# Optimization experiments

Hardware: AMD Instinct MI355X
Metric: run time of the kernel (lower is better)

The kernel has to match this reference:

```python
import jax, jax.numpy as jnp
import numpy as np

N = 100000          # nodes
DEG = 32            # fixed in-degree (every node has a non-empty mailbox)
E = N * DEG         # edges
IN_DIM = 25         # node feature dim; 3 aggregators * 1 scaler * 25 = 75
OUT_DIM = 128
AGG_EPS = 1e-5      # PNA std aggregator epsilon
BN_EPS = 1e-5       # BatchNorm1d epsilon


def setup_inputs() -> dict:
    key = jax.random.key(0)
    k = jax.random.split(key, 6)
    h = jax.random.normal(k[0], (N, IN_DIM), dtype=jnp.float32)
    snorm_n = jax.random.uniform(k[1], (N, 1), dtype=jnp.float32)
    # every node appears exactly DEG times as a destination -> degree 32
    edge_dst = jnp.repeat(jnp.arange(N, dtype=jnp.int32), DEG)
    edge_src = jax.random.randint(k[2], (E,), 0, N, dtype=jnp.int32)
    # posttrans MLP (1 layer): Linear(75 -> 128), no final activation
    W = jax.random.normal(k[3], (3 * IN_DIM, OUT_DIM), dtype=jnp.float32) / np.sqrt(3 * IN_DIM)
    b = jnp.zeros((OUT_DIM,), dtype=jnp.float32)
    # BatchNorm1d affine params
    gamma = jnp.ones((OUT_DIM,), dtype=jnp.float32)
    beta = jnp.zeros((OUT_DIM,), dtype=jnp.float32)
    return {"h": h, "snorm_n": snorm_n, "edge_src": edge_src, "edge_dst": edge_dst,
            "W": W, "b": b, "gamma": gamma, "beta": beta}


def reference(h, snorm_n, edge_src, edge_dst, W, b, gamma, beta):
    # --- message: e = src node features (pretrans_edges + message_func) ---
    e = h[edge_src]                                   # [E, IN_DIM] irregular gather
    # --- reduce: mean / max / std over each destination's mailbox ---
    ones = jnp.ones((e.shape[0],), dtype=h.dtype)
    deg = jax.ops.segment_sum(ones, edge_dst, num_segments=N)
    deg = jnp.maximum(deg, 1.0)[:, None]              # [N, 1]
    s1 = jax.ops.segment_sum(e, edge_dst, num_segments=N)
    mean = s1 / deg                                   # aggregate_mean
    mx = jax.ops.segment_max(e, edge_dst, num_segments=N)  # aggregate_max
    s2 = jax.ops.segment_sum(e * e, edge_dst, num_segments=N)
    var = jax.nn.relu(s2 / deg - mean * mean)         # aggregate_var
    std = jnp.sqrt(var + AGG_EPS)                     # aggregate_std
    agg = jnp.concatenate([mean, mx, std], axis=1)    # [N, 75]; identity scaler only
    # --- posttrans MLP: single Linear(75 -> 128), last_activation='none' ---
    z = agg @ W + b                                   # [N, OUT_DIM]
    # --- graph norm ---
    z = z * snorm_n
    # --- BatchNorm1d (training mode: batch statistics, biased variance) ---
    mu = jnp.mean(z, axis=0)
    v = jnp.var(z, axis=0)
    z = (z - mu) / jnp.sqrt(v + BN_EPS) * gamma + beta
    # --- relu; residual disabled (in_dim != out_dim); dropout p=0.0 is no-op ---
    return jax.nn.relu(z)
```

## Files before the change

### kernel.cpp

```cpp
#include <hip/hip_runtime.h>
#include <hip/hip_bf16.h>

#define NN 100000
#define DEG 32
#define IN_DIM 25
#define AGG_DIM 75
#define KPAD 104
#define OUT_DIM 128
#define NPB 10
#define NCHUNK (NN / NPB)
#define BLK 256
#define GRID 2048

typedef __attribute__((ext_vector_type(8))) short short8;
typedef __attribute__((ext_vector_type(4))) float f32x4;

static __device__ __forceinline__ ushort f2bf(float x) {
    __hip_bfloat16 h = __float2bfloat16(x);
    return *reinterpret_cast<ushort*>(&h);
}
static __device__ __forceinline__ float bf2f(ushort u) {
    return __uint_as_float(((unsigned)u) << 16);
}

__global__ __launch_bounds__(BLK) void prep(const float4* __restrict__ h4,
                                            ushort4* __restrict__ hb4,
                                            float* __restrict__ bnbuf) {
    int i = blockIdx.x * BLK + threadIdx.x;
    if (i < 2 * OUT_DIM) bnbuf[i] = 0.0f;
    const int total = NN * IN_DIM / 4;
    for (; i < total; i += GRID * BLK) {
        float4 v = h4[i];
        ushort4 o;
        o.x = f2bf(v.x); o.y = f2bf(v.y); o.z = f2bf(v.z); o.w = f2bf(v.w);
        hb4[i] = o;
    }
}

__global__ __launch_bounds__(BLK) void pna_main(
    const ushort* __restrict__ hb, const float* __restrict__ snorm,
    const int* __restrict__ esrc, const float* __restrict__ W,
    const float* __restrict__ b, float* __restrict__ z,
    float* __restrict__ bnbuf)
{
    __shared__ ushort agg[16][KPAD];

    const int t = threadIdx.x;
    const int lane = t & 63;
    const int wv = t >> 6;

    for (int i = t; i < 16 * KPAD; i += BLK) ((ushort*)agg)[i] = 0;

    const int cb0 = (wv * 2 + 0) * 16 + (lane & 15);
    const int cb1 = (wv * 2 + 1) * 16 + (lane & 15);
    short8 bfrag[2][3];
    #pragma unroll
    for (int ct = 0; ct < 2; ++ct) {
        const int cb = ct ? cb1 : cb0;
        #pragma unroll
        for (int kt = 0; kt < 3; ++kt) {
            short8 fr;
            #pragma unroll
            for (int j = 0; j < 8; ++j) {
                const int k = kt * 32 + ((lane >> 4) * 8) + j;
                const float w = (k < AGG_DIM) ? W[k * OUT_DIM + cb] : 0.0f;
                fr[j] = (short)f2bf(w);
            }
            bfrag[ct][kt] = fr;
        }
    }
    const float bb0 = b[cb0], bb1 = b[cb1];

    const int nl = t / IN_DIM;
    const int f  = t - nl * IN_DIM;
    const bool aggthread = (t < NPB * IN_DIM);

    float bns0 = 0.f, bnq0 = 0.f, bns1 = 0.f, bnq1 = 0.f;

    for (int chunk = blockIdx.x; chunk < NCHUNK; chunk += GRID) {
        const int n0 = chunk * NPB;
        __syncthreads();
        if (aggthread) {
            const int4* e4 = reinterpret_cast<const int4*>(esrc + (n0 + nl) * DEG);
            float s = 0.f, q = 0.f, m = -3.4e38f;
            #pragma unroll
            for (int eo = 0; eo < DEG / 4; ++eo) {
                const int4 ee = e4[eo];
                float v0 = bf2f(hb[ee.x * IN_DIM + f]);
                float v1 = bf2f(hb[ee.y * IN_DIM + f]);
                float v2 = bf2f(hb[ee.z * IN_DIM + f]);
                float v3 = bf2f(hb[ee.w * IN_DIM + f]);
                s += v0 + v1 + v2 + v3;
                q = fmaf(v0, v0, q); q = fmaf(v1, v1, q);
                q = fmaf(v2, v2, q); q = fmaf(v3, v3, q);
                m = fmaxf(m, fmaxf(fmaxf(v0, v1), fmaxf(v2, v3)));
            }
            const float mean = s * (1.0f / DEG);
            const float var  = fmaxf(q * (1.0f / DEG) - mean * mean, 0.0f);
            agg[nl][f]              = f2bf(mean);
            agg[nl][IN_DIM + f]     = f2bf(m);
            agg[nl][2 * IN_DIM + f] = f2bf(sqrtf(var + 1e-5f));
        }
        __syncthreads();

        const int arow = lane & 15;
        const int ak0  = (lane >> 4) * 8;
        f32x4 acc0 = {0.f, 0.f, 0.f, 0.f}, acc1 = {0.f, 0.f, 0.f, 0.f};
        #pragma unroll
        for (int kt = 0; kt < 3; ++kt) {
            const short8 afrag = *reinterpret_cast<const short8*>(&agg[arow][kt * 32 + ak0]);
            acc0 = __builtin_amdgcn_mfma_f32_16x16x32_bf16(afrag, bfrag[0][kt], acc0, 0, 0, 0);
            acc1 = __builtin_amdgcn_mfma_f32_16x16x32_bf16(afrag, bfrag[1][kt], acc1, 0, 0, 0);
        }
        const int r0 = (lane >> 4) * 4;
        #pragma unroll
        for (int r = 0; r < 4; ++r) {
            const int row = r0 + r;
            if (row < NPB) {
                const int node = n0 + row;
                const float sn = snorm[node];
                const float v0 = (acc0[r] + bb0) * sn;
                const float v1 = (acc1[r] + bb1) * sn;
                z[node * OUT_DIM + cb0] = v0;
                z[node * OUT_DIM + cb1] = v1;
                bns0 += v0; bnq0 = fmaf(v0, v0, bnq0);
                bns1 += v1; bnq1 = fmaf(v1, v1, bnq1);
            }
        }
    }

    bns0 += __shfl_xor(bns0, 16); bnq0 += __shfl_xor(bnq0, 16);
    bns0 += __shfl_xor(bns0, 32); bnq0 += __shfl_xor(bnq0, 32);
    bns1 += __shfl_xor(bns1, 16); bnq1 += __shfl_xor(bnq1, 16);
    bns1 += __shfl_xor(bns1, 32); bnq1 += __shfl_xor(bnq1, 32);
    if ((lane >> 4) == 0) {
        atomicAdd(&bnbuf[cb0], bns0);
        atomicAdd(&bnbuf[OUT_DIM + cb0], bnq0);
        atomicAdd(&bnbuf[cb1], bns1);
        atomicAdd(&bnbuf[OUT_DIM + cb1], bnq1);
    }
}

__global__ __launch_bounds__(BLK) void bn_apply(
    const float* __restrict__ bnbuf, const float* __restrict__ gamma,
    const float* __restrict__ beta, float* __restrict__ z)
{
    __shared__ float sc_s[OUT_DIM], sh_s[OUT_DIM];
    const int t = threadIdx.x;
    if (t < OUT_DIM) {
        const float mu = bnbuf[t] * (1.0f / NN);
        const float v  = fmaxf(bnbuf[OUT_DIM + t] * (1.0f / NN) - mu * mu, 0.0f);
        const float sc = gamma[t] * rsqrtf(v + 1e-5f);
        sc_s[t] = sc;
        sh_s[t] = beta[t] - mu * sc;
    }
    __syncthreads();
    const int c4 = (t & 31) * 4;
    const float s0 = sc_s[c4], s1 = sc_s[c4+1], s2 = sc_s[c4+2], s3 = sc_s[c4+3];
    const float h0 = sh_s[c4], h1 = sh_s[c4+1], h2 = sh_s[c4+2], h3 = sh_s[c4+3];

    float4* z4 = (float4*)z;
    const int total4 = NN * (OUT_DIM / 4);
    for (int i = blockIdx.x * BLK + t; i < total4; i += gridDim.x * BLK) {
        float4 v = z4[i];
        v.x = fmaxf(fmaf(v.x, s0, h0), 0.f);
        v.y = fmaxf(fmaf(v.y, s1, h1), 0.f);
        v.z = fmaxf(fmaf(v.z, s2, h2), 0.f);
        v.w = fmaxf(fmaf(v.w, s3, h3), 0.f);
        z4[i] = v;
    }
}

extern "C" void kernel_launch(void* const* d_in, const int* in_sizes, int n_in,
                              void* d_out, int out_size, void* d_ws, size_t ws_size,
                              hipStream_t stream) {
    const float* h     = (const float*)d_in[0];
    const float* snorm = (const float*)d_in[1];
    const int*   esrc  = (const int*)d_in[2];
    const float* W     = (const float*)d_in[4];
    const float* b     = (const float*)d_in[5];
    const float* gamma = (const float*)d_in[6];
    const float* beta  = (const float*)d_in[7];
    float*  z     = (float*)d_out;
    float*  bnbuf = (float*)d_ws;
    ushort* hb    = (ushort*)((char*)d_ws + 1024);

    prep<<<GRID, BLK, 0, stream>>>((const float4*)h, (ushort4*)hb, bnbuf);
    pna_main<<<GRID, BLK, 0, stream>>>(hb, snorm, esrc, W, b, z, bnbuf);
    bn_apply<<<GRID, BLK, 0, stream>>>(bnbuf, gamma, beta, z);
}
```

Measured before the change: 192.4 us.

## Pad bf16 node rows to 64B and gather via global_load_lds

The prep kernel now writes each node's bf16 features into a padded 64-byte row, so the gather in the main kernel can fetch whole rows with 16-byte direct global-to-LDS loads (global_load_lds) using XOR-swizzled placement. This replaces the previous scattered 2-byte per-feature gathers. Each block now handles 16 nodes per chunk, which fills the 16-row MFMA tile and removes the row guard. Threads reduce two packed features per LDS word with rotated edge order to avoid bank conflicts. The padded copy uses more workspace and bandwidth, and the larger LDS footprint may lower occupancy.

```diff
diff --git a/kernel.cpp b/kernel.cpp
--- a/kernel.cpp
+++ b/kernel.cpp
@@ -7,33 +7,47 @@
 #define AGG_DIM 75
 #define KPAD 104
 #define OUT_DIM 128
-#define NPB 10
+#define NPB 16
+#define EPC (NPB * DEG)
 #define NCHUNK (NN / NPB)
 #define BLK 256
 #define GRID 2048
+#define PREP_GRID 391
 
 typedef __attribute__((ext_vector_type(8))) short short8;
 typedef __attribute__((ext_vector_type(4))) float f32x4;
 
-static __device__ __forceinline__ ushort f2bf(float x) {
+static __device__ __forceinline__ unsigned f2bf(float x) {
     __hip_bfloat16 h = __float2bfloat16(x);
-    return *reinterpret_cast<ushort*>(&h);
-}
-static __device__ __forceinline__ float bf2f(ushort u) {
-    return __uint_as_float(((unsigned)u) << 16);
-}
-
-__global__ __launch_bounds__(BLK) void prep(const float4* __restrict__ h4,
-                                            ushort4* __restrict__ hb4,
+    return (unsigned)*reinterpret_cast<unsigned short*>(&h);
+}
+static __device__ __forceinline__ float bflo(unsigned v) { return __uint_as_float(v << 16); }
+static __device__ __forceinline__ float bfhi(unsigned v) { return __uint_as_float(v & 0xffff0000u); }
+
+static __device__ __forceinline__ void gload16(const void* g, void* l) {
+    __builtin_amdgcn_global_load_lds(
+        (const __attribute__((address_space(1))) unsigned*)g,
+        (__attribute__((address_space(3))) unsigned*)l, 16, 0, 0);
+}
+
+__global__ __launch_bounds__(BLK) void prep(const float* __restrict__ h,
+                                            ushort* __restrict__ hbp,
                                             float* __restrict__ bnbuf) {
-    int i = blockIdx.x * BLK + threadIdx.x;
-    if (i < 2 * OUT_DIM) bnbuf[i] = 0.0f;
-    const int total = NN * IN_DIM / 4;
-    for (; i < total; i += GRID * BLK) {
-        float4 v = h4[i];
-        ushort4 o;
-        o.x = f2bf(v.x); o.y = f2bf(v.y); o.z = f2bf(v.z); o.w = f2bf(v.w);
-        hb4[i] = o;
+    const int t = threadIdx.x;
+    const int gid = blockIdx.x * BLK + t;
+    if (gid < 2 * OUT_DIM) bnbuf[gid] = 0.0f;
+    for (int n = gid; n < NN; n += PREP_GRID * BLK) {
+        const float* row = h + n * IN_DIM;
+        unsigned u[16];
+        #pragma unroll
+        for (int k = 0; k < 12; ++k) u[k] = f2bf(row[2 * k]) | (f2bf(row[2 * k + 1]) << 16);
+        u[12] = f2bf(row[24]);
+        u[13] = 0u; u[14] = 0u; u[15] = 0u;
+        uint4* dst = (uint4*)(hbp + (size_t)n * 32);
+        dst[0] = make_uint4(u[0], u[1], u[2], u[3]);
+        dst[1] = make_uint4(u[4], u[5], u[6], u[7]);
+        dst[2] = make_uint4(u[8], u[9], u[10], u[11]);
+        dst[3] = make_uint4(u[12], u[13], u[14], u[15]);
     }
 }
 
@@ -43,13 +57,15 @@
     const float* __restrict__ b, float* __restrict__ z,
     float* __restrict__ bnbuf)
 {
-    __shared__ ushort agg[16][KPAD];
+    __shared__ __align__(1024) ushort E_s[EPC][32];
+    __shared__ int    ids_s[EPC];
+    __shared__ ushort agg[NPB][KPAD];
 
     const int t = threadIdx.x;
     const int lane = t & 63;
     const int wv = t >> 6;
 
-    for (int i = t; i < 16 * KPAD; i += BLK) ((ushort*)agg)[i] = 0;
+    for (int i = t; i < NPB * KPAD; i += BLK) ((ushort*)agg)[i] = 0;
 
     const int cb0 = (wv * 2 + 0) * 16 + (lane & 15);
     const int cb1 = (wv * 2 + 1) * 16 + (lane & 15);
@@ -71,35 +87,57 @@
     }
     const float bb0 = b[cb0], bb1 = b[cb1];
 
-    const int nl = t / IN_DIM;
-    const int f  = t - nl * IN_DIM;
-    const bool aggthread = (t < NPB * IN_DIM);
+    const int lsub = lane >> 2;
+    const int prt  = lane & 3;
+    const int nl2 = t >> 4;
+    const int f2  = t & 15;
+    const bool a2act = (f2 < 13);
+    const int dcol = f2 ^ ((nl2 & 3) << 2);
 
     float bns0 = 0.f, bnq0 = 0.f, bns1 = 0.f, bnq1 = 0.f;
 
     for (int chunk = blockIdx.x; chunk < NCHUNK; chunk += GRID) {
         const int n0 = chunk * NPB;
+
+        ((int2*)ids_s)[t] = ((const int2*)(esrc + n0 * DEG))[t];
         __syncthreads();
-        if (aggthread) {
-            const int4* e4 = reinterpret_cast<const int4*>(esrc + (n0 + nl) * DEG);
-            float s = 0.f, q = 0.f, m = -3.4e38f;
+
+        #pragma unroll
+        for (int i = 0; i < 8; ++i) {
+            const int g = wv * 8 + i;
+            const int r = g * 16 + lsub;
+            const int src = ids_s[r];
+            const int psrc = prt ^ ((r >> 5) & 3);
+            gload16((const char*)hb + ((size_t)src << 6) + (psrc << 4),
+                    (char*)E_s + (g << 10));
+        }
+        __syncthreads();
+
+        if (a2act) {
+            const unsigned* Ew = (const unsigned*)E_s;
+            const unsigned base = (unsigned)(nl2 * 512 + dcol);
+            float s0 = 0.f, q0 = 0.f, m0 = -3.4e38f;
+            float s1 = 0.f, q1 = 0.f, m1 = -3.4e38f;
             #pragma unroll
-            for (int eo = 0; eo < DEG / 4; ++eo) {
-                const int4 ee = e4[eo];
-                float v0 = bf2f(hb[ee.x * IN_DIM + f]);
-                float v1 = bf2f(hb[ee.y * IN_DIM + f]);
-                float v2 = bf2f(hb[ee.z * IN_DIM + f]);
-                float v3 = bf2f(hb[ee.w * IN_DIM + f]);
-                s += v0 + v1 + v2 + v3;
-                q = fmaf(v0, v0, q); q = fmaf(v1, v1, q);
-                q = fmaf(v2, v2, q); q = fmaf(v3, v3, q);
-                m = fmaxf(m, fmaxf(fmaxf(v0, v1), fmaxf(v2, v3)));
+            for (int e = 0; e < 32; ++e) {
+                const int ee = (e + nl2) & 31;
+                const unsigned v = Ew[base + ee * 16];
+                const float lo = bflo(v), hi = bfhi(v);
+                s0 += lo; q0 = fmaf(lo, lo, q0); m0 = fmaxf(m0, lo);
+                s1 += hi; q1 = fmaf(hi, hi, q1); m1 = fmaxf(m1, hi);
             }
-            const float mean = s * (1.0f / DEG);
-            const float var  = fmaxf(q * (1.0f / DEG) - mean * mean, 0.0f);
-            agg[nl][f]              = f2bf(mean);
-            agg[nl][IN_DIM + f]     = f2bf(m);
-            agg[nl][2 * IN_DIM + f] = f2bf(sqrtf(var + 1e-5f));
+            const float inv = 1.0f / DEG;
+            const float mean0 = s0 * inv, var0 = fmaxf(q0 * inv - mean0 * mean0, 0.f);
+            const float mean1 = s1 * inv, var1 = fmaxf(q1 * inv - mean1 * mean1, 0.f);
+            const int ff = f2 * 2;
+            agg[nl2][ff]              = (ushort)f2bf(mean0);
+            agg[nl2][IN_DIM + ff]     = (ushort)f2bf(m0);
+            agg[nl2][2 * IN_DIM + ff] = (ushort)f2bf(sqrtf(var0 + 1e-5f));
+            if (ff + 1 < IN_DIM) {
+                agg[nl2][ff + 1]              = (ushort)f2bf(mean1);
+                agg[nl2][IN_DIM + ff + 1]     = (ushort)f2bf(m1);
+                agg[nl2][2 * IN_DIM + ff + 1] = (ushort)f2bf(sqrtf(var1 + 1e-5f));
+            }
         }
         __syncthreads();
 
@@ -108,24 +146,21 @@
         f32x4 acc0 = {0.f, 0.f, 0.f, 0.f}, acc1 = {0.f, 0.f, 0.f, 0.f};
         #pragma unroll
         for (int kt = 0; kt < 3; ++kt) {
-            const short8 afrag = *reinterpret_cast<const short8*>(&agg[arow][kt * 32 + ak0]);
-            acc0 = __builtin_amdgcn_mfma_f32_16x16x32_bf16(afrag, bfrag[0][kt], acc0, 0, 0, 0);
-            acc1 = __builtin_amdgcn_mfma_f32_16x16x32_bf16(afrag, bfrag[1][kt], acc1, 0, 0, 0);
+            const short8 af = *reinterpret_cast<const short8*>(&agg[arow][kt * 32 + ak0]);
+            acc0 = __builtin_amdgcn_mfma_f32_16x16x32_bf16(af, bfrag[0][kt], acc0, 0, 0, 0);
+            acc1 = __builtin_amdgcn_mfma_f32_16x16x32_bf16(af, bfrag[1][kt], acc1, 0, 0, 0);
         }
         const int r0 = (lane >> 4) * 4;
         #pragma unroll
         for (int r = 0; r < 4; ++r) {
-            const int row = r0 + r;
-            if (row < NPB) {
-                const int node = n0 + row;
-                const float sn = snorm[node];
-                const float v0 = (acc0[r] + bb0) * sn;
-                const float v1 = (acc1[r] + bb1) * sn;
-                z[node * OUT_DIM + cb0] = v0;
-                z[node * OUT_DIM + cb1] = v1;
-                bns0 += v0; bnq0 = fmaf(v0, v0, bnq0);
-                bns1 += v1; bnq1 = fmaf(v1, v1, bnq1);
-            }
+            const int node = n0 + r0 + r;
+            const float sn = snorm[node];
+            const float v0 = (acc0[r] + bb0) * sn;
+            const float v1 = (acc1[r] + bb1) * sn;
+            z[node * OUT_DIM + cb0] = v0;
+            z[node * OUT_DIM + cb1] = v1;
+            bns0 += v0; bnq0 = fmaf(v0, v0, bnq0);
+            bns1 += v1; bnq1 = fmaf(v1, v1, bnq1);
         }
     }
 
@@ -183,9 +218,9 @@
     const float* beta  = (const float*)d_in[7];
     float*  z     = (float*)d_out;
     float*  bnbuf = (float*)d_ws;
-    ushort* hb    = (ushort*)((char*)d_ws + 1024);
-
-    prep<<<GRID, BLK, 0, stream>>>((const float4*)h, (ushort4*)hb, bnbuf);
-    pna_main<<<GRID, BLK, 0, stream>>>(hb, snorm, esrc, W, b, z, bnbuf);
-    bn_apply<<<GRID, BLK, 0, stream>>>(bnbuf, gamma, beta, z);
-}
+    ushort* hbp   = (ushort*)((char*)d_ws + 1024);
+
+    prep<<<PREP_GRID, BLK, 0, stream>>>(h, hbp, bnbuf);
+    pna_main<<<GRID, BLK, 0, stream>>>(hbp, snorm, esrc, W, b, z, bnbuf);
+    bn_apply<<<2048, BLK, 0, stream>>>(bnbuf, gamma, beta, z);
+}
```

Result: faster. 186.2 us (-3.2%).
